# Optimization experiments

Measured on AMD Instinct MI355X. Metric: run time of the kernel, lower is better.

## Reference

```python
import jax, jax.numpy as jnp
import numpy as np
import math

S, D = 8192, 128

def setup_inputs() -> dict:
    key = jax.random.key(0)
    kq, kk, kv = jax.random.split(key, 3)
    return {
        "q": jax.random.normal(kq, (S, D), dtype=jnp.float32),
        "k": jax.random.normal(kk, (S, D), dtype=jnp.float32),
        "v": jax.random.normal(kv, (S, D), dtype=jnp.float32),
    }

def reference(q, k, v):
    # scores: [S, S]; scale by sqrt(d) as in the torch module
    scale = 1.0 / math.sqrt(q.shape[1])
    scores = (q @ k.T) * scale
    attn = jax.nn.softmax(scores, axis=-1)
    return attn @ v
```

## Files before the change

kernel.cpp:

```cpp
#include <hip/hip_runtime.h>
#include <hip/hip_bf16.h>

#define SEQ 8192
#define HD 128
#define BM 256
#define BN 64
#define NQT (SEQ / BM)
#define THREADS 512

typedef __bf16 bf16_t;
typedef __bf16 bf16x2 __attribute__((ext_vector_type(2)));
typedef __bf16 bf16x8 __attribute__((ext_vector_type(8)));
typedef float f32x4 __attribute__((ext_vector_type(4)));
typedef float f32x16 __attribute__((ext_vector_type(16)));
typedef unsigned int u32x4 __attribute__((ext_vector_type(4)));

#if __has_builtin(__builtin_amdgcn_exp2f)
__device__ inline float exp2_fast(float x) { return __builtin_amdgcn_exp2f(x); }
#else
__device__ inline float exp2_fast(float x) { return exp2f(x); }
#endif

__device__ inline void load_lds16(const void* g, void* l) {
  __builtin_amdgcn_global_load_lds(
      (const __attribute__((address_space(1))) void*)g,
      (__attribute__((address_space(3))) void*)l, 16, 0, 0);
}

__global__ __launch_bounds__(256) void prep_kernel(const float* __restrict__ K,
                                                   const float* __restrict__ V,
                                                   bf16_t* __restrict__ Kb,
                                                   bf16_t* __restrict__ VT) {
  const int b = (int)blockIdx.x;
  const int tid = (int)threadIdx.x;
  if (b < 256) {
    __shared__ float tile[64][65];
    const int T = b & 127;
    const int d0 = (b >> 7) * 64;
    const int s0 = T * 64;
    const int r = tid >> 2;
    const int c0 = (tid & 3) * 16;
#pragma unroll
    for (int j4 = 0; j4 < 4; ++j4) {
      float4 x = *(const float4*)&V[(size_t)(s0 + r) * HD + d0 + c0 + j4 * 4];
      tile[r][c0 + j4 * 4 + 0] = x.x;
      tile[r][c0 + j4 * 4 + 1] = x.y;
      tile[r][c0 + j4 * 4 + 2] = x.z;
      tile[r][c0 + j4 * 4 + 3] = x.w;
    }
    __syncthreads();
    const int d_l = tid & 63;
    const int kc0 = (tid >> 6) * 2;
#pragma unroll
    for (int k2 = 0; k2 < 2; ++k2) {
      const int kc = kc0 + k2;
      bf16x8 wv;
#pragma unroll
      for (int j = 0; j < 8; ++j) wv[j] = (bf16_t)tile[kc * 8 + j][d_l];
      *(bf16x8*)&VT[((size_t)(T * 8 + kc) * 128 + d0 + d_l) * 8] = wv;
    }
  } else {
    const int base = (b - 256) * 2048 + tid * 8;
    const int row = base >> 7;
    const int c = (base >> 3) & 15;
    const int T = row >> 6;
    const int r = row & 63;
    float4 a = *(const float4*)&K[base];
    float4 cc = *(const float4*)&K[base + 4];
    bf16x8 f;
    f[0] = (bf16_t)a.x; f[1] = (bf16_t)a.y; f[2] = (bf16_t)a.z; f[3] = (bf16_t)a.w;
    f[4] = (bf16_t)cc.x; f[5] = (bf16_t)cc.y; f[6] = (bf16_t)cc.z; f[7] = (bf16_t)cc.w;
    *(bf16x8*)&Kb[((size_t)(T * 16 + c) * 64 + r) * 8] = f;
  }
}

__global__ __launch_bounds__(THREADS, 2) void fattn_kernel(
    const float* __restrict__ Q, const bf16_t* __restrict__ Kb,
    const bf16_t* __restrict__ VT, float* __restrict__ Opart,
    float* __restrict__ Lpart, int kshift, int nit) {
  __shared__ __align__(16) bf16_t kt2[2][16][64][8];
  __shared__ __align__(16) bf16_t vt2[2][8][128][8];

  const int tid = (int)threadIdx.x;
  const int lane = tid & 63;
  const int w = tid >> 6;
  const int h = lane >> 5;
  const int n32 = lane & 31;

  const int qt = (int)blockIdx.x >> kshift;
  const int sp = (int)blockIdx.x & ((1 << kshift) - 1);
  const int qbase = qt * BM;
  const int tile0 = sp * nit;

  const float SC2 = 0.08838834764831845f * 1.4426950408889634f;

  bf16x8 qf[8];
  {
    const float* qp = Q + (size_t)(qbase + w * 32 + n32) * HD + h * 8;
#pragma unroll
    for (int kk = 0; kk < 8; ++kk) {
      float4 a = *(const float4*)(qp + kk * 16);
      float4 b = *(const float4*)(qp + kk * 16 + 4);
      bf16x8 f;
      f[0] = (bf16_t)(a.x * SC2); f[1] = (bf16_t)(a.y * SC2);
      f[2] = (bf16_t)(a.z * SC2); f[3] = (bf16_t)(a.w * SC2);
      f[4] = (bf16_t)(b.x * SC2); f[5] = (bf16_t)(b.y * SC2);
      f[6] = (bf16_t)(b.z * SC2); f[7] = (bf16_t)(b.w * SC2);
      qf[kk] = f;
    }
  }

  f32x16 o_acc[4];
#pragma unroll
  for (int i = 0; i < 4; ++i)
#pragma unroll
    for (int e = 0; e < 16; ++e) o_acc[i][e] = 0.f;
  float l_acc = 0.f;

  const int rr0 = w * 2;

#pragma unroll
  for (int t = 0; t < 2; ++t) {
    const int rr = rr0 + t;
    load_lds16(Kb + ((size_t)(tile0 * 16 + rr) * 64 + lane) * 8,
               (char*)&kt2[0][0][0][0] + rr * 1024);
    load_lds16(VT + ((size_t)(tile0 * 8 + (rr >> 1)) * 128 + (rr & 1) * 64 + lane) * 8,
               (char*)&vt2[0][0][0][0] + rr * 1024);
  }
  __syncthreads();

  for (int it = 0; it < nit; ++it) {
    const int cur = it & 1;
    const int nxt = cur ^ 1;
    const int ntile = tile0 + ((it + 1 < nit) ? it + 1 : 0);
#pragma unroll
    for (int t = 0; t < 2; ++t) {
      const int rr = rr0 + t;
      load_lds16(Kb + ((size_t)(ntile * 16 + rr) * 64 + lane) * 8,
                 (char*)&kt2[nxt][0][0][0] + rr * 1024);
      load_lds16(VT + ((size_t)(ntile * 8 + (rr >> 1)) * 128 + (rr & 1) * 64 + lane) * 8,
                 (char*)&vt2[nxt][0][0][0] + rr * 1024);
    }

    bf16x8 pa[4];
#pragma unroll
    for (int kg = 0; kg < 2; ++kg) {
      f32x16 sacc;
#pragma unroll
      for (int e = 0; e < 16; ++e) sacc[e] = 0.f;
#pragma unroll
      for (int kk = 0; kk < 8; ++kk) {
        bf16x8 af = *(const bf16x8*)&kt2[cur][2 * kk + h][kg * 32 + n32][0];
        sacc = __builtin_amdgcn_mfma_f32_32x32x16_bf16(af, qf[kk], sacc, 0, 0, 0);
      }
#pragma unroll
      for (int kk2 = 0; kk2 < 2; ++kk2) {
        float pf[8];
#pragma unroll
        for (int j = 0; j < 8; ++j) pf[j] = exp2_fast(sacc[8 * kk2 + j]);
        l_acc += ((pf[0] + pf[1]) + (pf[2] + pf[3])) +
                 ((pf[4] + pf[5]) + (pf[6] + pf[7]));
        bf16x2 p0, p1, p2, p3;
        p0[0] = (bf16_t)pf[0]; p0[1] = (bf16_t)pf[1];
        p1[0] = (bf16_t)pf[2]; p1[1] = (bf16_t)pf[3];
        p2[0] = (bf16_t)pf[4]; p2[1] = (bf16_t)pf[5];
        p3[0] = (bf16_t)pf[6]; p3[1] = (bf16_t)pf[7];
        const unsigned int sA = __builtin_bit_cast(unsigned int, p0);
        const unsigned int sB = __builtin_bit_cast(unsigned int, p1);
        const unsigned int sC = __builtin_bit_cast(unsigned int, p2);
        const unsigned int sD = __builtin_bit_cast(unsigned int, p3);
        unsigned int s0 = h ? sA : sC, s1 = h ? sB : sD;
        unsigned int r0 = __shfl_xor(s0, 32);
        unsigned int r1 = __shfl_xor(s1, 32);
        unsigned int o0 = h ? sC : sA, o1 = h ? sD : sB;
        u32x4 fv;
        fv[0] = h ? r0 : o0; fv[1] = h ? r1 : o1;
        fv[2] = h ? o0 : r0; fv[3] = h ? o1 : r1;
        pa[kg * 2 + kk2] = __builtin_bit_cast(bf16x8, fv);
      }
    }

#pragma unroll
    for (int C = 0; C < 4; ++C) {
#pragma unroll
      for (int ot = 0; ot < 4; ++ot) {
        bf16x8 vb = *(const bf16x8*)&vt2[cur][C * 2 + h][ot * 32 + n32][0];
        o_acc[ot] = __builtin_amdgcn_mfma_f32_32x32x16_bf16(pa[C], vb, o_acc[ot], 0, 0, 0);
      }
    }

    __syncthreads();
  }

  {
    float* op = Opart + ((size_t)sp * SEQ + qbase + w * 32) * HD;
#pragma unroll
    for (int ot = 0; ot < 4; ++ot)
#pragma unroll
      for (int reg = 0; reg < 16; ++reg) {
        const int row = (reg & 3) + 8 * (reg >> 2) + 4 * h;
        op[row * HD + ot * 32 + n32] = o_acc[ot][reg];
      }
    float l = l_acc + __shfl_xor(l_acc, 32);
    if (lane < 32)
      Lpart[(size_t)sp * SEQ + qbase + w * 32 + n32] = l;
  }
}

__global__ __launch_bounds__(256) void combine_kernel(const float* __restrict__ Opart,
                                                      const float* __restrict__ Lpart,
                                                      float* __restrict__ out, int ksplit) {
  const int tid = (int)threadIdx.x;
  const int row = (int)blockIdx.x * 8 + (tid >> 5);
  const int c0 = (tid & 31) * 4;
  float lsum = 0.f;
  for (int s = 0; s < ksplit; ++s) lsum += Lpart[(size_t)s * SEQ + row];
  f32x4 acc;
#pragma unroll
  for (int e = 0; e < 4; ++e) acc[e] = 0.f;
  for (int s = 0; s < ksplit; ++s) {
    f32x4 o = *(const f32x4*)&Opart[((size_t)s * SEQ + row) * HD + c0];
#pragma unroll
    for (int e = 0; e < 4; ++e) acc[e] += o[e];
  }
  const float inv = 1.0f / lsum;
  f32x4 res;
#pragma unroll
  for (int e = 0; e < 4; ++e) res[e] = acc[e] * inv;
  *(f32x4*)&out[(size_t)row * HD + c0] = res;
}

extern "C" void kernel_launch(void* const* d_in, const int* in_sizes, int n_in,
                              void* d_out, int out_size, void* d_ws, size_t ws_size,
                              hipStream_t stream) {
  const float* Q = (const float*)d_in[0];
  const float* K = (const float*)d_in[1];
  const float* V = (const float*)d_in[2];
  float* out = (float*)d_out;

  int ksplit = 8, kshift = 3;
  while (ksplit > 1) {
    size_t need = (size_t)ksplit * SEQ * HD * 4
                + (size_t)ksplit * SEQ * 4
                + (size_t)SEQ * HD * 2 * 2;
    if (need <= ws_size) break;
    ksplit >>= 1; kshift--;
  }

  char* ws = (char*)d_ws;
  float* Opart = (float*)ws;
  float* Lpart = (float*)(ws + (size_t)ksplit * SEQ * HD * 4);
  bf16_t* Kb = (bf16_t*)(ws + (size_t)ksplit * SEQ * HD * 4 + (size_t)ksplit * SEQ * 4);
  bf16_t* VT = Kb + (size_t)SEQ * HD;

  const int nit = SEQ / (ksplit * BN);

  prep_kernel<<<768, 256, 0, stream>>>(K, V, Kb, VT);
  fattn_kernel<<<NQT * ksplit, THREADS, 0, stream>>>(Q, Kb, VT, Opart, Lpart, kshift, nit);
  combine_kernel<<<SEQ / 8, 256, 0, stream>>>(Opart, Lpart, out, ksplit);
}
```

Before: 116.6 us.

## Software-pipeline QK^T of next tile with PV of previous tile

Restructures the attention loop so each iteration issues the QK^T MFMAs for the current K tile together with the PV MFMAs for the previous tile's probabilities, and only then runs exp and packing. This lets the matrix-core work overlap with the exp/shuffle work. V gets a triple-buffered LDS ring so the delayed PV step can still read its tile while the next one is prefetched. It also adds s_setprio around the MFMA sections, peels the first and last iterations, and stops issuing the redundant prefetch on the final tile. In exchange it uses more LDS and more registers for the two probability buffers, and the peeled structure appears to assume an even iteration count.

Measured after the change: 113.7 us. -2.5%, faster.

```diff
diff --git a/kernel.cpp b/kernel.cpp
--- a/kernel.cpp
+++ b/kernel.cpp
@@ -79,7 +79,7 @@
     const bf16_t* __restrict__ VT, float* __restrict__ Opart,
     float* __restrict__ Lpart, int kshift, int nit) {
   __shared__ __align__(16) bf16_t kt2[2][16][64][8];
-  __shared__ __align__(16) bf16_t vt2[2][8][128][8];
+  __shared__ __align__(16) bf16_t vt3[3][8][128][8];
 
   const int tid = (int)threadIdx.x;
   const int lane = tid & 63;
@@ -117,7 +117,77 @@
     for (int e = 0; e < 16; ++e) o_acc[i][e] = 0.f;
   float l_acc = 0.f;
 
+  bf16x8 paA[4], paB[4];
+
   const int rr0 = w * 2;
+
+#define EXPPACK(SACC, KG, PDST)                                            \
+  _Pragma("unroll")                                                        \
+  for (int kk2 = 0; kk2 < 2; ++kk2) {                                      \
+    float pf[8];                                                           \
+    _Pragma("unroll")                                                      \
+    for (int j = 0; j < 8; ++j) pf[j] = exp2_fast(SACC[8 * kk2 + j]);      \
+    l_acc += ((pf[0] + pf[1]) + (pf[2] + pf[3])) +                         \
+             ((pf[4] + pf[5]) + (pf[6] + pf[7]));                          \
+    bf16x2 p0, p1, p2, p3;                                                 \
+    p0[0] = (bf16_t)pf[0]; p0[1] = (bf16_t)pf[1];                          \
+    p1[0] = (bf16_t)pf[2]; p1[1] = (bf16_t)pf[3];                          \
+    p2[0] = (bf16_t)pf[4]; p2[1] = (bf16_t)pf[5];                          \
+    p3[0] = (bf16_t)pf[6]; p3[1] = (bf16_t)pf[7];                          \
+    const unsigned int sA = __builtin_bit_cast(unsigned int, p0);          \
+    const unsigned int sB = __builtin_bit_cast(unsigned int, p1);          \
+    const unsigned int sC = __builtin_bit_cast(unsigned int, p2);          \
+    const unsigned int sD = __builtin_bit_cast(unsigned int, p3);          \
+    unsigned int s0 = h ? sA : sC, s1 = h ? sB : sD;                       \
+    unsigned int r0 = __shfl_xor(s0, 32);                                  \
+    unsigned int r1 = __shfl_xor(s1, 32);                                  \
+    unsigned int o0 = h ? sC : sA, o1 = h ? sD : sB;                       \
+    u32x4 fv;                                                              \
+    fv[0] = h ? r0 : o0; fv[1] = h ? r1 : o1;                              \
+    fv[2] = h ? o0 : r0; fv[3] = h ? o1 : r1;                              \
+    PDST[(KG) * 2 + kk2] = __builtin_bit_cast(bf16x8, fv);                 \
+  }
+
+#define FBODY(IT, PPREV, PCUR, KC)                                         \
+  {                                                                        \
+    const int it_ = (IT);                                                  \
+    if (it_ + 1 < nit) {                                                   \
+      const int ntile = tile0 + it_ + 1;                                   \
+      _Pragma("unroll")                                                    \
+      for (int t = 0; t < 2; ++t) {                                        \
+        const int rr = rr0 + t;                                            \
+        load_lds16(Kb + ((size_t)(ntile * 16 + rr) * 64 + lane) * 8,       \
+                   (char*)&kt2[(KC) ^ 1][0][0][0] + rr * 1024);            \
+        load_lds16(VT + ((size_t)(ntile * 8 + (rr >> 1)) * 128 + (rr & 1) * 64 + lane) * 8, \
+                   (char*)&vt3[vd][0][0][0] + rr * 1024);                  \
+      }                                                                    \
+    }                                                                      \
+    f32x16 sacc0, sacc1;                                                   \
+    _Pragma("unroll")                                                      \
+    for (int e = 0; e < 16; ++e) { sacc0[e] = 0.f; sacc1[e] = 0.f; }       \
+    __builtin_amdgcn_s_setprio(1);                                         \
+    _Pragma("unroll")                                                      \
+    for (int kk = 0; kk < 8; ++kk) {                                       \
+      bf16x8 af0 = *(const bf16x8*)&kt2[KC][2 * kk + h][n32][0];           \
+      sacc0 = __builtin_amdgcn_mfma_f32_32x32x16_bf16(af0, qf[kk], sacc0, 0, 0, 0); \
+      bf16x8 af1 = *(const bf16x8*)&kt2[KC][2 * kk + h][32 + n32][0];      \
+      sacc1 = __builtin_amdgcn_mfma_f32_32x32x16_bf16(af1, qf[kk], sacc1, 0, 0, 0); \
+    }                                                                      \
+    _Pragma("unroll")                                                      \
+    for (int C = 0; C < 4; ++C) {                                          \
+      _Pragma("unroll")                                                    \
+      for (int ot = 0; ot < 4; ++ot) {                                     \
+        bf16x8 vb = *(const bf16x8*)&vt3[vp][C * 2 + h][ot * 32 + n32][0]; \
+        o_acc[ot] = __builtin_amdgcn_mfma_f32_32x32x16_bf16(PPREV[C], vb, o_acc[ot], 0, 0, 0); \
+      }                                                                    \
+    }                                                                      \
+    __builtin_amdgcn_s_setprio(0);                                         \
+    EXPPACK(sacc0, 0, PCUR)                                                \
+    EXPPACK(sacc1, 1, PCUR)                                                \
+    vp = (vp + 1 == 3) ? 0 : vp + 1;                                       \
+    vd = (vd + 1 == 3) ? 0 : vd + 1;                                       \
+    __syncthreads();                                                       \
+  }
 
 #pragma unroll
   for (int t = 0; t < 2; ++t) {
@@ -125,72 +195,61 @@
     load_lds16(Kb + ((size_t)(tile0 * 16 + rr) * 64 + lane) * 8,
                (char*)&kt2[0][0][0][0] + rr * 1024);
     load_lds16(VT + ((size_t)(tile0 * 8 + (rr >> 1)) * 128 + (rr & 1) * 64 + lane) * 8,
-               (char*)&vt2[0][0][0][0] + rr * 1024);
+               (char*)&vt3[0][0][0][0] + rr * 1024);
   }
   __syncthreads();
 
-  for (int it = 0; it < nit; ++it) {
-    const int cur = it & 1;
-    const int nxt = cur ^ 1;
-    const int ntile = tile0 + ((it + 1 < nit) ? it + 1 : 0);
-#pragma unroll
-    for (int t = 0; t < 2; ++t) {
-      const int rr = rr0 + t;
-      load_lds16(Kb + ((size_t)(ntile * 16 + rr) * 64 + lane) * 8,
-                 (char*)&kt2[nxt][0][0][0] + rr * 1024);
-      load_lds16(VT + ((size_t)(ntile * 8 + (rr >> 1)) * 128 + (rr & 1) * 64 + lane) * 8,
-                 (char*)&vt2[nxt][0][0][0] + rr * 1024);
-    }
-
-    bf16x8 pa[4];
-#pragma unroll
-    for (int kg = 0; kg < 2; ++kg) {
-      f32x16 sacc;
-#pragma unroll
-      for (int e = 0; e < 16; ++e) sacc[e] = 0.f;
-#pragma unroll
-      for (int kk = 0; kk < 8; ++kk) {
-        bf16x8 af = *(const bf16x8*)&kt2[cur][2 * kk + h][kg * 32 + n32][0];
-        sacc = __builtin_amdgcn_mfma_f32_32x32x16_bf16(af, qf[kk], sacc, 0, 0, 0);
+  {
+    if (nit > 1) {
+      const int ntile = tile0 + 1;
+#pragma unroll
+      for (int t = 0; t < 2; ++t) {
+        const int rr = rr0 + t;
+        load_lds16(Kb + ((size_t)(ntile * 16 + rr) * 64 + lane) * 8,
+                   (char*)&kt2[1][0][0][0] + rr * 1024);
+        load_lds16(VT + ((size_t)(ntile * 8 + (rr >> 1)) * 128 + (rr & 1) * 64 + lane) * 8,
+                   (char*)&vt3[1][0][0][0] + rr * 1024);
       }
-#pragma unroll
-      for (int kk2 = 0; kk2 < 2; ++kk2) {
-        float pf[8];
-#pragma unroll
-        for (int j = 0; j < 8; ++j) pf[j] = exp2_fast(sacc[8 * kk2 + j]);
-        l_acc += ((pf[0] + pf[1]) + (pf[2] + pf[3])) +
-                 ((pf[4] + pf[5]) + (pf[6] + pf[7]));
-        bf16x2 p0, p1, p2, p3;
-        p0[0] = (bf16_t)pf[0]; p0[1] = (bf16_t)pf[1];
-        p1[0] = (bf16_t)pf[2]; p1[1] = (bf16_t)pf[3];
-        p2[0] = (bf16_t)pf[4]; p2[1] = (bf16_t)pf[5];
-        p3[0] = (bf16_t)pf[6]; p3[1] = (bf16_t)pf[7];
-        const unsigned int sA = __builtin_bit_cast(unsigned int, p0);
-        const unsigned int sB = __builtin_bit_cast(unsigned int, p1);
-        const unsigned int sC = __builtin_bit_cast(unsigned int, p2);
-        const unsigned int sD = __builtin_bit_cast(unsigned int, p3);
-        unsigned int s0 = h ? sA : sC, s1 = h ? sB : sD;
-        unsigned int r0 = __shfl_xor(s0, 32);
-        unsigned int r1 = __shfl_xor(s1, 32);
-        unsigned int o0 = h ? sC : sA, o1 = h ? sD : sB;
-        u32x4 fv;
-        fv[0] = h ? r0 : o0; fv[1] = h ? r1 : o1;
-        fv[2] = h ? o0 : r0; fv[3] = h ? o1 : r1;
-        pa[kg * 2 + kk2] = __builtin_bit_cast(bf16x8, fv);
-      }
-    }
-
-#pragma unroll
-    for (int C = 0; C < 4; ++C) {
-#pragma unroll
-      for (int ot = 0; ot < 4; ++ot) {
-        bf16x8 vb = *(const bf16x8*)&vt2[cur][C * 2 + h][ot * 32 + n32][0];
-        o_acc[ot] = __builtin_amdgcn_mfma_f32_32x32x16_bf16(pa[C], vb, o_acc[ot], 0, 0, 0);
-      }
-    }
-
+    }
+    f32x16 sacc0, sacc1;
+#pragma unroll
+    for (int e = 0; e < 16; ++e) { sacc0[e] = 0.f; sacc1[e] = 0.f; }
+    __builtin_amdgcn_s_setprio(1);
+#pragma unroll
+    for (int kk = 0; kk < 8; ++kk) {
+      bf16x8 af0 = *(const bf16x8*)&kt2[0][2 * kk + h][n32][0];
+      sacc0 = __builtin_amdgcn_mfma_f32_32x32x16_bf16(af0, qf[kk], sacc0, 0, 0, 0);
+      bf16x8 af1 = *(const bf16x8*)&kt2[0][2 * kk + h][32 + n32][0];
+      sacc1 = __builtin_amdgcn_mfma_f32_32x32x16_bf16(af1, qf[kk], sacc1, 0, 0, 0);
+    }
+    __builtin_amdgcn_s_setprio(0);
+    EXPPACK(sacc0, 0, paA)
+    EXPPACK(sacc1, 1, paA)
     __syncthreads();
   }
+
+  int vp = 0;
+  int vd = 2;
+
+  for (int it = 1; it + 1 <= nit - 1; it += 2) {
+    FBODY(it, paA, paB, 1)
+    FBODY(it + 1, paB, paA, 0)
+  }
+  FBODY(nit - 1, paA, paB, 1)
+
+  __builtin_amdgcn_s_setprio(1);
+#pragma unroll
+  for (int C = 0; C < 4; ++C) {
+#pragma unroll
+    for (int ot = 0; ot < 4; ++ot) {
+      bf16x8 vb = *(const bf16x8*)&vt3[vp][C * 2 + h][ot * 32 + n32][0];
+      o_acc[ot] = __builtin_amdgcn_mfma_f32_32x32x16_bf16(paB[C], vb, o_acc[ot], 0, 0, 0);
+    }
+  }
+  __builtin_amdgcn_s_setprio(0);
+
+#undef FBODY
+#undef EXPPACK
 
   {
     float* op = Opart + ((size_t)sp * SEQ + qbase + w * 32) * HD;
```
